# Performance work log

Hardware: AMD Instinct MI355X
Metric: run time of the kernel (lower is better)

Reference implementation:

```python
import jax, jax.numpy as jnp
import numpy as np
from jax import lax

B, T, C = 32, 512, 128
K = 3                      # top_k periods
MIN_P, MAX_P = 8, 64       # period search band
P_MAX = MAX_P              # grid width
CYC_MAX = (T + MIN_P - 1) // MIN_P
KW = 9                     # cyc-axis depthwise kernel
GN_G = 32                  # _best_gn_groups(128)
EPS_GN = 1e-5
EPS_ORTH = 1e-6
EPS_W = 1e-8


def setup_inputs() -> dict:
    key = jax.random.key(0)
    ks = jax.random.split(key, 4)
    return {
        "x": jax.random.normal(ks[0], (B, T, C), jnp.float32),
        "W_dw": jax.random.normal(ks[1], (C, 1, KW), jnp.float32) * 0.1,
        "W_pw": jax.random.normal(ks[2], (C, C), jnp.float32) * (1.0 / np.sqrt(C)),
        "gn_weight": jnp.ones((C,), jnp.float32),
        "gn_bias": jnp.zeros((C,), jnp.float32),
        "W_gate": jax.random.normal(ks[3], (C, C), jnp.float32) * (1.0 / np.sqrt(C)),
        "gamma": jnp.full((C,), 1e-3, jnp.float32),
    }


def _autocorr_topk(x):
    # x: [B,T,C] -> period idx [B,K], softmax weights [B,K]
    Xf = jnp.fft.rfft(x, axis=1)
    Pm = (Xf * jnp.conj(Xf)).real.mean(-1)          # [B, T//2+1]
    r = jnp.fft.irfft(Pm, n=T, axis=1)              # [B, T] autocorrelation
    lag = jnp.arange(T)
    valid = (lag >= MIN_P) & (lag <= MAX_P)
    very_neg = jnp.finfo(x.dtype).min / 8
    rm = jnp.where(valid[None, :], r, very_neg)
    vals, idx = lax.top_k(rm, K)
    w = jax.nn.softmax(vals, axis=1)
    return idx, w


def _fold(s, p):
    # s: [N,T,C], p: [N] int periods -> Z [N,C,CYC_MAX,P_MAX], mask, unfold index maps
    N = s.shape[0]
    p = jnp.maximum(p, 1)
    tpad = ((T + p - 1) // p) * p                   # [N]
    cyc = jnp.arange(CYC_MAX)[None, :, None]
    pos = jnp.arange(P_MAX)[None, None, :]
    time = cyc * p[:, None, None] + pos             # [N,CYC_MAX,P_MAX]
    valid = (pos < p[:, None, None]) & (time < tpad[:, None, None])
    # right-side reflect padding indices
    m = 2 * (T - 1)
    rr = time % m
    src_idx = jnp.where(rr < T, rr, m - rr)
    src = jnp.take_along_axis(s, src_idx.reshape(N, -1)[:, :, None], axis=1)
    src = src.reshape(N, CYC_MAX, P_MAX, C) * valid[..., None].astype(s.dtype)
    Z = jnp.transpose(src, (0, 3, 1, 2))            # [N,C,CYC_MAX,P_MAX]
    mask2d = valid[:, None].astype(s.dtype)         # [N,1,CYC_MAX,P_MAX]
    t = jnp.arange(T)[None, :]
    cyc_T = jnp.clip(t // p[:, None], 0, CYC_MAX - 1)
    pos_T = jnp.clip(t % p[:, None], 0, P_MAX - 1)
    return Z, mask2d, cyc_T, pos_T


def _cyc_conv(Z, mask2d, W_dw, W_pw, gn_w, gn_b, W_gate, gamma):
    # CycAxisConv1d: mean over period axis, depthwise+pointwise conv along cyc,
    # GroupNorm, GELU, SE-gate, LayerScale residual broadcast back to 2D.
    N, _, L, _ = Z.shape
    u = Z.mean(-1)                                  # [N,C,L]
    h = lax.conv_general_dilated(u, W_dw, (1,), [(KW // 2, KW // 2)],
                                 dimension_numbers=('NCH', 'OIH', 'NCH'),
                                 feature_group_count=C)
    h = jnp.einsum('oc,ncl->nol', W_pw, h)
    hg = h.reshape(N, GN_G, C // GN_G, L)
    mean = hg.mean((2, 3), keepdims=True)
    var = hg.var((2, 3), keepdims=True)
    hg = (hg - mean) * lax.rsqrt(var + EPS_GN)
    h = hg.reshape(N, C, L) * gn_w[None, :, None] + gn_b[None, :, None]
    h = jax.nn.gelu(h, approximate=False)
    gate = jax.nn.sigmoid(jnp.einsum('oc,nc->no', W_gate, u.mean(-1)))
    h = h * gate[:, :, None]
    x2d = h[..., None] * gamma[None, :, None, None] * mask2d
    return Z + x2d


def _unfold(Z, cyc_T, pos_T):
    N = Z.shape[0]
    Zf = Z.reshape(N, C, CYC_MAX * P_MAX)
    sp = jnp.clip(cyc_T * P_MAX + pos_T, 0, CYC_MAX * P_MAX - 1)  # [N,T]
    y = jnp.take_along_axis(Zf, sp[:, None, :], axis=2)           # [N,C,T]
    return jnp.transpose(y, (0, 2, 1))                            # [N,T,C]


def reference(x, W_dw, W_pw, gn_weight, gn_bias, W_gate, gamma):
    idx, w = _autocorr_topk(x)                      # [B,K], [B,K]
    p_flat = idx.reshape(-1)                        # [B*K]
    s = jnp.repeat(x, K, axis=0)                    # [B*K,T,C]
    Z, mask2d, cyc_T, pos_T = _fold(s, p_flat)
    Z = _cyc_conv(Z, mask2d, W_dw, W_pw, gn_weight, gn_bias, W_gate, gamma)
    y = _unfold(Z, cyc_T, pos_T).reshape(B, K, T, C)
    periodic = jnp.einsum('bk,bktc->btc', w, y)
    # period confidence Gamma from weight entropy
    H = -(w * jnp.log(w + EPS_W)).sum(1)
    Gamma = jnp.clip(1.0 - H / (jnp.log(float(K) + EPS_W) + EPS_W), 0.0, 1.0)
    # orthogonal residual of local part against periodic part
    local = x - periodic
    num = (local * periodic).sum(1, keepdims=True)
    den = (periodic * periodic).sum(1, keepdims=True) + EPS_ORTH
    local_orth = local - num / den * periodic
    g = Gamma[:, None, None]
    return g * (periodic + local_orth) + (1.0 - g) * x
```

## Files before the change

### kernel.cpp

```cpp
#include <hip/hip_runtime.h>
#include <math.h>

static constexpr int Bn   = 32;
static constexpr int Tn   = 512;
static constexpr int Cn   = 128;
static constexpr int Kk   = 3;
static constexpr int NLAG = 57;
static constexpr int CYC  = 64;
static constexpr int KWn  = 9;

__global__ __launch_bounds__(256) void k_autocorr(const float* __restrict__ x,
    float* __restrict__ r_ws) {
  const int b   = blockIdx.x >> 3;
  const int grp = blockIdx.x & 7;
  const int L0  = 8 + grp * 8;
  const int tid = threadIdx.x;
  const float4* X4 = (const float4*)(x + (size_t)b * Tn * Cn);

  float acc[8];
#pragma unroll
  for (int i = 0; i < 8; ++i) acc[i] = 0.f;

  for (int it = 0; it < 8; ++it) {
    const int id = it * 256 + tid;
    const int c4 = id & 31;
    const int t0 = (id >> 5) * 8;
    float4 A[8];
#pragma unroll
    for (int j = 0; j < 8; ++j) A[j] = X4[(t0 + j) * 32 + c4];
    float4 R[16];
#pragma unroll
    for (int j = 0; j < 16; ++j) R[j] = X4[((t0 + L0 + j) & 511) * 32 + c4];
#pragma unroll
    for (int g = 0; g < 8; ++g) {
#pragma unroll
      for (int j = 0; j < 8; ++j) {
        const float4 a = A[j];
        const float4 r = R[g + j];
        acc[g] += a.x * r.x + a.y * r.y + a.z * r.z + a.w * r.w;
      }
    }
  }

  __shared__ float lds_r[4][8];
  const int lane = tid & 63, wave = tid >> 6;
#pragma unroll
  for (int g = 0; g < 8; ++g) {
    float v = acc[g];
#pragma unroll
    for (int m = 32; m > 0; m >>= 1) v += __shfl_xor(v, m, 64);
    if (lane == 0) lds_r[wave][g] = v;
  }
  __syncthreads();
  if (tid < 8) {
    const int li = grp * 8 + tid;
    if (li < NLAG) {
      r_ws[b * NLAG + li] =
          (lds_r[0][tid] + lds_r[1][tid] + lds_r[2][tid] + lds_r[3][tid]) * (1.0f / Cn);
    }
  }
}

__global__ __launch_bounds__(64) void k_topk(const float* __restrict__ r_ws,
    int* __restrict__ p_idx, float* __restrict__ wv, float* __restrict__ gval) {
  const int b = blockIdx.x;
  const int tid = threadIdx.x;
  __shared__ float rs[NLAG];
  if (tid < NLAG) rs[tid] = r_ws[b * NLAG + tid];
  __syncthreads();
  if (tid == 0) {
    float tmp[NLAG];
    for (int i = 0; i < NLAG; ++i) tmp[i] = rs[i];
    float vals[Kk]; int lags[Kk];
    for (int k = 0; k < Kk; ++k) {
      float best = -INFINITY; int bi = 0;
      for (int i = 0; i < NLAG; ++i)
        if (tmp[i] > best) { best = tmp[i]; bi = i; }
      vals[k] = best; lags[k] = bi + 8; tmp[bi] = -INFINITY;
    }
    const float m  = vals[0];
    const float e0 = expf(vals[0] - m), e1 = expf(vals[1] - m), e2 = expf(vals[2] - m);
    const float s  = e0 + e1 + e2;
    const float w0 = e0 / s, w1 = e1 / s, w2 = e2 / s;
    p_idx[b * 3 + 0] = lags[0]; p_idx[b * 3 + 1] = lags[1]; p_idx[b * 3 + 2] = lags[2];
    wv[b * 3 + 0] = w0; wv[b * 3 + 1] = w1; wv[b * 3 + 2] = w2;
    const float H  = -(w0 * logf(w0 + 1e-8f) + w1 * logf(w1 + 1e-8f) + w2 * logf(w2 + 1e-8f));
    const float lg = logf(3.0f + 1e-8f) + 1e-8f;
    float G = 1.0f - H / lg;
    gval[b] = fminf(fmaxf(G, 0.0f), 1.0f);
  }
}

__global__ __launch_bounds__(128) void k_fold_u(const float* __restrict__ x,
    const int* __restrict__ p_idx, float* __restrict__ u) {
  const int l = blockIdx.x;
  const int n = blockIdx.y;
  const int c = threadIdx.x;
  const int p = p_idx[n];
  const int ncyc = (Tn + p - 1) / p;
  float acc = 0.f;
  if (l < ncyc) {
    const float* xb = x + (size_t)(n / 3) * Tn * Cn;
    const int base = l * p;
    for (int j = 0; j < p; ++j) {
      const int time = base + j;
      const int src = time < Tn ? time : (2 * (Tn - 1) - time);
      acc += xb[src * Cn + c];
    }
  }
  u[((size_t)n * CYC + l) * Cn + c] = acc * (1.0f / 64.0f);
}

__global__ __launch_bounds__(256) void k_cycconv(
    const float* __restrict__ u, const float* __restrict__ Wdw,
    const float* __restrict__ Wpw, const float* __restrict__ gnw,
    const float* __restrict__ gnb, const float* __restrict__ Wgate,
    float* __restrict__ hh) {
  const int n  = blockIdx.x;
  const int og = blockIdx.y;
  const int tid = threadIdx.x;
  const int l  = tid & 63;
  const int wq = __builtin_amdgcn_readfirstlane(tid >> 6);

  __shared__ float smem[8320];
  __shared__ float ubar_s[Cn];
  __shared__ float gates_s[16];

  const float* un = u + (size_t)n * CYC * Cn;

  for (int i = 0; i < 32; ++i) {
    const int idx = i * 256 + tid;
    const int ll = idx >> 7, cc = idx & 127;
    smem[ll * 129 + cc] = un[idx];
  }
  __syncthreads();

  if (tid < Cn) {
    float s = 0.f;
    for (int ll = 0; ll < CYC; ++ll) s += smem[ll * 129 + tid];
    ubar_s[tid] = s * (1.0f / CYC);
  }

  float hreg[32];
  {
    const int c0 = wq * 32;
#pragma unroll
    for (int i = 0; i < 32; ++i) {
      const int c = c0 + i;
      float s = 0.f;
#pragma unroll
      for (int k = 0; k < KWn; ++k) {
        const int ll = l + k - KWn / 2;
        if (ll >= 0 && ll < CYC) s += smem[ll * 129 + c] * Wdw[c * KWn + k];
      }
      hreg[i] = s;
    }
  }
  __syncthreads();

  if (tid < 16) {
    const int o = og * 16 + tid;
    float z = 0.f;
    for (int c = 0; c < Cn; ++c) z += Wgate[o * Cn + c] * ubar_s[c];
    gates_s[tid] = 1.0f / (1.0f + expf(-z));
  }

  {
    const int c0 = wq * 32;
#pragma unroll
    for (int i = 0; i < 32; ++i) smem[(c0 + i) * 65 + l] = hreg[i];
  }
  __syncthreads();

  const int o4 = og * 16 + wq * 4;
  float acc[4];
#pragma unroll
  for (int i = 0; i < 4; ++i) acc[i] = 0.f;
  const float* wb = Wpw + (size_t)o4 * Cn;
  for (int c = 0; c < Cn; ++c) {
    const float hv = smem[c * 65 + l];
#pragma unroll
    for (int i = 0; i < 4; ++i) acc[i] = fmaf(wb[i * Cn + c], hv, acc[i]);
  }

  float s1 = acc[0] + acc[1] + acc[2] + acc[3];
  float s2 = acc[0]*acc[0] + acc[1]*acc[1] + acc[2]*acc[2] + acc[3]*acc[3];
#pragma unroll
  for (int m = 32; m > 0; m >>= 1) {
    s1 += __shfl_xor(s1, m, 64);
    s2 += __shfl_xor(s2, m, 64);
  }
  const float mean = s1 * (1.0f / 256.0f);
  const float var  = s2 * (1.0f / 256.0f) - mean * mean;
  const float rstd = rsqrtf(var + 1e-5f);

  float4 res;
  float* rp = (float*)&res;
#pragma unroll
  for (int i = 0; i < 4; ++i) {
    const int o = o4 + i;
    float h = (acc[i] - mean) * rstd;
    h = h * gnw[o] + gnb[o];
    h = 0.5f * h * (1.0f + erff(h * 0.70710678118654752440f));
    rp[i] = h * gates_s[o - og * 16];
  }
  *(float4*)(hh + (size_t)n * CYC * Cn + l * Cn + o4) = res;
}

__global__ __launch_bounds__(128) void k_dot(const float* __restrict__ x,
    const float* __restrict__ hh, const int* __restrict__ p_idx,
    const float* __restrict__ wv, const float* __restrict__ gamma,
    float* __restrict__ pna, float* __restrict__ pda) {
  const int q = blockIdx.x, b = blockIdx.y;
  const int tid = threadIdx.x;
  const int t0 = q * 64;
  __shared__ unsigned short cycs[64][4];

  const int p0 = p_idx[b * 3 + 0], p1 = p_idx[b * 3 + 1], p2 = p_idx[b * 3 + 2];
  const float w0 = wv[b * 3 + 0], w1 = wv[b * 3 + 1], w2 = wv[b * 3 + 2];
  const float sw = w0 + w1 + w2;
  if (tid < 64) {
    const int t = t0 + tid;
    cycs[tid][0] = (unsigned short)(t / p0);
    cycs[tid][1] = (unsigned short)(t / p1);
    cycs[tid][2] = (unsigned short)(t / p2);
  }
  __syncthreads();

  const int c = tid;
  const float gam = gamma[c];
  const float* hh0 = hh + ((size_t)(b * 3 + 0) * CYC) * Cn + c;
  const float* hh1 = hh + ((size_t)(b * 3 + 1) * CYC) * Cn + c;
  const float* hh2 = hh + ((size_t)(b * 3 + 2) * CYC) * Cn + c;
  const float* xb = x + (size_t)b * Tn * Cn;

  float na = 0.f, da = 0.f;
  for (int tt = 0; tt < 64; ++tt) {
    const int t = t0 + tt;
    const float xv = xb[t * Cn + c];
    const float dv = gam * (w0 * hh0[cycs[tt][0] * Cn] +
                            w1 * hh1[cycs[tt][1] * Cn] +
                            w2 * hh2[cycs[tt][2] * Cn]);
    const float P = sw * xv + dv;
    na += (xv - P) * P;
    da += P * P;
  }
  pna[((size_t)b * 8 + q) * Cn + c] = na;
  pda[((size_t)b * 8 + q) * Cn + c] = da;
}

__global__ __launch_bounds__(128) void k_out(const float* __restrict__ x,
    const float* __restrict__ hh, const int* __restrict__ p_idx,
    const float* __restrict__ wv, const float* __restrict__ gval,
    const float* __restrict__ gamma, const float* __restrict__ pna,
    const float* __restrict__ pda, float* __restrict__ out) {
  const int q = blockIdx.x, b = blockIdx.y;
  const int tid = threadIdx.x;
  const int t0 = q * 64;
  __shared__ unsigned short cycs[64][4];

  const int p0 = p_idx[b * 3 + 0], p1 = p_idx[b * 3 + 1], p2 = p_idx[b * 3 + 2];
  const float w0 = wv[b * 3 + 0], w1 = wv[b * 3 + 1], w2 = wv[b * 3 + 2];
  const float sw = w0 + w1 + w2;
  const float g = gval[b];
  if (tid < 64) {
    const int t = t0 + tid;
    cycs[tid][0] = (unsigned short)(t / p0);
    cycs[tid][1] = (unsigned short)(t / p1);
    cycs[tid][2] = (unsigned short)(t / p2);
  }
  __syncthreads();

  const int c = tid;
  float num = 0.f, den = 1e-6f;
#pragma unroll
  for (int qq = 0; qq < 8; ++qq) {
    num += pna[((size_t)b * 8 + qq) * Cn + c];
    den += pda[((size_t)b * 8 + qq) * Cn + c];
  }
  const float sc = g * (num / den);

  const float gam = gamma[c];
  const float* hh0 = hh + ((size_t)(b * 3 + 0) * CYC) * Cn + c;
  const float* hh1 = hh + ((size_t)(b * 3 + 1) * CYC) * Cn + c;
  const float* hh2 = hh + ((size_t)(b * 3 + 2) * CYC) * Cn + c;
  const float* xb = x + (size_t)b * Tn * Cn;
  float* ob = out + (size_t)b * Tn * Cn;

  for (int tt = 0; tt < 64; ++tt) {
    const int t = t0 + tt;
    const float xv = xb[t * Cn + c];
    const float dv = gam * (w0 * hh0[cycs[tt][0] * Cn] +
                            w1 * hh1[cycs[tt][1] * Cn] +
                            w2 * hh2[cycs[tt][2] * Cn]);
    const float P = sw * xv + dv;
    ob[t * Cn + c] = xv - sc * P;
  }
}

extern "C" void kernel_launch(void* const* d_in, const int* in_sizes, int n_in,
                              void* d_out, int out_size, void* d_ws, size_t ws_size,
                              hipStream_t stream) {
  const float* x     = (const float*)d_in[0];
  const float* Wdw   = (const float*)d_in[1];
  const float* Wpw   = (const float*)d_in[2];
  const float* gnw   = (const float*)d_in[3];
  const float* gnb   = (const float*)d_in[4];
  const float* Wgate = (const float*)d_in[5];
  const float* gamma = (const float*)d_in[6];
  float* out = (float*)d_out;

  char* ws = (char*)d_ws;
  int*   p_idx = (int*)ws;
  float* wvp   = (float*)(ws + 512);
  float* gvalp = (float*)(ws + 1024);
  float* r_ws  = (float*)(ws + 2048);
  float* pna   = (float*)(ws + 10240);
  float* pda   = (float*)(ws + 10240 + 131072);
  float* u     = (float*)(ws + 10240 + 262144);
  float* hh    = (float*)(ws + 10240 + 262144 + 3145728);

  k_autocorr<<<Bn * 8, 256, 0, stream>>>(x, r_ws);
  k_topk<<<Bn, 64, 0, stream>>>(r_ws, p_idx, wvp, gvalp);
  k_fold_u<<<dim3(CYC, Bn * Kk), 128, 0, stream>>>(x, p_idx, u);
  k_cycconv<<<dim3(Bn * Kk, 8), 256, 0, stream>>>(u, Wdw, Wpw, gnw, gnb, Wgate, hh);
  k_dot<<<dim3(8, Bn), 128, 0, stream>>>(x, hh, p_idx, wvp, gamma, pna, pda);
  k_out<<<dim3(8, Bn), 128, 0, stream>>>(x, hh, p_idx, wvp, gvalp, gamma, pna, pda, out);
}
```

Before: 165.0 us.

## Fuse topk and fold into consumers, split autocorr over time for more blocks

```diff
diff --git a/kernel.cpp b/kernel.cpp
--- a/kernel.cpp
+++ b/kernel.cpp
@@ -9,10 +9,35 @@
 static constexpr int CYC  = 64;
 static constexpr int KWn  = 9;
 
-__global__ __launch_bounds__(256) void k_autocorr(const float* __restrict__ x,
+__device__ __forceinline__ void topk_scan(const float* __restrict__ r_ws, int b,
+    int& p0, int& p1, int& p2, float& w0, float& w1, float& w2, float& Gv) {
+  const float* r0 = r_ws + (size_t)(b * 4 + 0) * NLAG;
+  const float* r1 = r_ws + (size_t)(b * 4 + 1) * NLAG;
+  const float* r2 = r_ws + (size_t)(b * 4 + 2) * NLAG;
+  const float* r3 = r_ws + (size_t)(b * 4 + 3) * NLAG;
+  float v0 = -INFINITY, v1 = -INFINITY, v2 = -INFINITY;
+  int i0 = 0, i1 = 0, i2 = 0;
+  for (int i = 0; i < NLAG; ++i) {
+    const float v = r0[i] + r1[i] + r2[i] + r3[i];
+    if (v > v0)      { v2 = v1; i2 = i1; v1 = v0; i1 = i0; v0 = v; i0 = i; }
+    else if (v > v1) { v2 = v1; i2 = i1; v1 = v; i1 = i; }
+    else if (v > v2) { v2 = v; i2 = i; }
+  }
+  p0 = i0 + 8; p1 = i1 + 8; p2 = i2 + 8;
+  const float e1 = expf(v1 - v0), e2 = expf(v2 - v0);
+  const float s = 1.0f + e1 + e2;
+  w0 = 1.0f / s; w1 = e1 / s; w2 = e2 / s;
+  const float H  = -(w0 * logf(w0 + 1e-8f) + w1 * logf(w1 + 1e-8f) + w2 * logf(w2 + 1e-8f));
+  const float lg = logf(3.0f + 1e-8f) + 1e-8f;
+  Gv = fminf(fmaxf(1.0f - H / lg, 0.0f), 1.0f);
+}
+
+__global__ __launch_bounds__(256, 3) void k_autocorr(const float* __restrict__ x,
     float* __restrict__ r_ws) {
-  const int b   = blockIdx.x >> 3;
-  const int grp = blockIdx.x & 7;
+  const int bk  = blockIdx.x;
+  const int b   = bk >> 5;
+  const int grp = (bk >> 2) & 7;
+  const int th  = bk & 3;
   const int L0  = 8 + grp * 8;
   const int tid = threadIdx.x;
   const float4* X4 = (const float4*)(x + (size_t)b * Tn * Cn);
@@ -21,8 +46,9 @@
 #pragma unroll
   for (int i = 0; i < 8; ++i) acc[i] = 0.f;
 
-  for (int it = 0; it < 8; ++it) {
-    const int id = it * 256 + tid;
+#pragma unroll
+  for (int s = 0; s < 2; ++s) {
+    const int id = (th * 2 + s) * 256 + tid;
     const int c4 = id & 31;
     const int t0 = (id >> 5) * 8;
     float4 A[8];
@@ -55,83 +81,53 @@
   if (tid < 8) {
     const int li = grp * 8 + tid;
     if (li < NLAG) {
-      r_ws[b * NLAG + li] =
+      r_ws[(size_t)(b * 4 + th) * NLAG + li] =
           (lds_r[0][tid] + lds_r[1][tid] + lds_r[2][tid] + lds_r[3][tid]) * (1.0f / Cn);
     }
   }
 }
 
-__global__ __launch_bounds__(64) void k_topk(const float* __restrict__ r_ws,
-    int* __restrict__ p_idx, float* __restrict__ wv, float* __restrict__ gval) {
-  const int b = blockIdx.x;
-  const int tid = threadIdx.x;
-  __shared__ float rs[NLAG];
-  if (tid < NLAG) rs[tid] = r_ws[b * NLAG + tid];
-  __syncthreads();
-  if (tid == 0) {
-    float tmp[NLAG];
-    for (int i = 0; i < NLAG; ++i) tmp[i] = rs[i];
-    float vals[Kk]; int lags[Kk];
-    for (int k = 0; k < Kk; ++k) {
-      float best = -INFINITY; int bi = 0;
-      for (int i = 0; i < NLAG; ++i)
-        if (tmp[i] > best) { best = tmp[i]; bi = i; }
-      vals[k] = best; lags[k] = bi + 8; tmp[bi] = -INFINITY;
-    }
-    const float m  = vals[0];
-    const float e0 = expf(vals[0] - m), e1 = expf(vals[1] - m), e2 = expf(vals[2] - m);
-    const float s  = e0 + e1 + e2;
-    const float w0 = e0 / s, w1 = e1 / s, w2 = e2 / s;
-    p_idx[b * 3 + 0] = lags[0]; p_idx[b * 3 + 1] = lags[1]; p_idx[b * 3 + 2] = lags[2];
-    wv[b * 3 + 0] = w0; wv[b * 3 + 1] = w1; wv[b * 3 + 2] = w2;
-    const float H  = -(w0 * logf(w0 + 1e-8f) + w1 * logf(w1 + 1e-8f) + w2 * logf(w2 + 1e-8f));
-    const float lg = logf(3.0f + 1e-8f) + 1e-8f;
-    float G = 1.0f - H / lg;
-    gval[b] = fminf(fmaxf(G, 0.0f), 1.0f);
-  }
-}
-
-__global__ __launch_bounds__(128) void k_fold_u(const float* __restrict__ x,
-    const int* __restrict__ p_idx, float* __restrict__ u) {
-  const int l = blockIdx.x;
-  const int n = blockIdx.y;
-  const int c = threadIdx.x;
-  const int p = p_idx[n];
-  const int ncyc = (Tn + p - 1) / p;
-  float acc = 0.f;
-  if (l < ncyc) {
-    const float* xb = x + (size_t)(n / 3) * Tn * Cn;
-    const int base = l * p;
-    for (int j = 0; j < p; ++j) {
-      const int time = base + j;
-      const int src = time < Tn ? time : (2 * (Tn - 1) - time);
-      acc += xb[src * Cn + c];
-    }
-  }
-  u[((size_t)n * CYC + l) * Cn + c] = acc * (1.0f / 64.0f);
-}
-
-__global__ __launch_bounds__(256) void k_cycconv(
-    const float* __restrict__ u, const float* __restrict__ Wdw,
+__global__ __launch_bounds__(256) void k_foldconv(const float* __restrict__ x,
+    const float* __restrict__ r_ws, const float* __restrict__ Wdw,
     const float* __restrict__ Wpw, const float* __restrict__ gnw,
     const float* __restrict__ gnb, const float* __restrict__ Wgate,
     float* __restrict__ hh) {
   const int n  = blockIdx.x;
   const int og = blockIdx.y;
+  const int b  = n / 3;
+  const int kk = n - b * 3;
   const int tid = threadIdx.x;
   const int l  = tid & 63;
-  const int wq = __builtin_amdgcn_readfirstlane(tid >> 6);
+
+  int p0, p1, p2; float w0, w1, w2, Gv;
+  topk_scan(r_ws, b, p0, p1, p2, w0, w1, w2, Gv);
+  const int p = (kk == 0) ? p0 : ((kk == 1) ? p1 : p2);
+  const int ncyc = (Tn + p - 1) / p;
 
   __shared__ float smem[8320];
   __shared__ float ubar_s[Cn];
   __shared__ float gates_s[16];
 
-  const float* un = u + (size_t)n * CYC * Cn;
-
-  for (int i = 0; i < 32; ++i) {
-    const int idx = i * 256 + tid;
-    const int ll = idx >> 7, cc = idx & 127;
-    smem[ll * 129 + cc] = un[idx];
+  const float4* X4 = (const float4*)(x + (size_t)b * Tn * Cn);
+  for (int it = 0; it < 8; ++it) {
+    const int id = it * 256 + tid;
+    const int c4 = id & 31;
+    const int ll = id >> 5;
+    float sx = 0.f, sy = 0.f, sz = 0.f, sw2 = 0.f;
+    if (ll < ncyc) {
+      const int base = ll * p;
+      for (int j = 0; j < p; ++j) {
+        const int time = base + j;
+        const int src = time < Tn ? time : (2 * (Tn - 1) - time);
+        const float4 a = X4[src * 32 + c4];
+        sx += a.x; sy += a.y; sz += a.z; sw2 += a.w;
+      }
+    }
+    const int adr = ll * 129 + c4 * 4;
+    smem[adr + 0] = sx * (1.0f / 64.0f);
+    smem[adr + 1] = sy * (1.0f / 64.0f);
+    smem[adr + 2] = sz * (1.0f / 64.0f);
+    smem[adr + 3] = sw2 * (1.0f / 64.0f);
   }
   __syncthreads();
 
@@ -142,40 +138,32 @@
   }
 
   float hreg[32];
-  {
-    const int c0 = wq * 32;
-#pragma unroll
-    for (int i = 0; i < 32; ++i) {
-      const int c = c0 + i;
-      float s = 0.f;
-#pragma unroll
-      for (int k = 0; k < KWn; ++k) {
-        const int ll = l + k - KWn / 2;
-        if (ll >= 0 && ll < CYC) s += smem[ll * 129 + c] * Wdw[c * KWn + k];
-      }
-      hreg[i] = s;
+  const int c0 = (tid >> 6) * 32;
+#pragma unroll
+  for (int i = 0; i < 32; ++i) {
+    const int c = c0 + i;
+    float s = 0.f;
+#pragma unroll
+    for (int k2 = 0; k2 < KWn; ++k2) {
+      const int ll = l + k2 - KWn / 2;
+      if (ll >= 0 && ll < CYC) s += smem[ll * 129 + c] * Wdw[c * KWn + k2];
     }
-  }
-  __syncthreads();
-
+    hreg[i] = s;
+  }
+  __syncthreads();
+
+#pragma unroll
+  for (int i = 0; i < 32; ++i) smem[(c0 + i) * 65 + l] = hreg[i];
   if (tid < 16) {
     const int o = og * 16 + tid;
     float z = 0.f;
     for (int c = 0; c < Cn; ++c) z += Wgate[o * Cn + c] * ubar_s[c];
     gates_s[tid] = 1.0f / (1.0f + expf(-z));
   }
-
-  {
-    const int c0 = wq * 32;
-#pragma unroll
-    for (int i = 0; i < 32; ++i) smem[(c0 + i) * 65 + l] = hreg[i];
-  }
-  __syncthreads();
-
-  const int o4 = og * 16 + wq * 4;
-  float acc[4];
-#pragma unroll
-  for (int i = 0; i < 4; ++i) acc[i] = 0.f;
+  __syncthreads();
+
+  const int o4 = og * 16 + (tid >> 6) * 4;
+  float acc[4] = {0.f, 0.f, 0.f, 0.f};
   const float* wb = Wpw + (size_t)o4 * Cn;
   for (int c = 0; c < Cn; ++c) {
     const float hv = smem[c * 65 + l];
@@ -204,20 +192,20 @@
     h = 0.5f * h * (1.0f + erff(h * 0.70710678118654752440f));
     rp[i] = h * gates_s[o - og * 16];
   }
-  *(float4*)(hh + (size_t)n * CYC * Cn + l * Cn + o4) = res;
+  *(float4*)(hh + ((size_t)n * CYC + l) * Cn + o4) = res;
 }
 
 __global__ __launch_bounds__(128) void k_dot(const float* __restrict__ x,
-    const float* __restrict__ hh, const int* __restrict__ p_idx,
-    const float* __restrict__ wv, const float* __restrict__ gamma,
-    float* __restrict__ pna, float* __restrict__ pda) {
+    const float* __restrict__ hh, const float* __restrict__ r_ws,
+    const float* __restrict__ gamma, float* __restrict__ pna,
+    float* __restrict__ pda) {
   const int q = blockIdx.x, b = blockIdx.y;
   const int tid = threadIdx.x;
   const int t0 = q * 64;
   __shared__ unsigned short cycs[64][4];
 
-  const int p0 = p_idx[b * 3 + 0], p1 = p_idx[b * 3 + 1], p2 = p_idx[b * 3 + 2];
-  const float w0 = wv[b * 3 + 0], w1 = wv[b * 3 + 1], w2 = wv[b * 3 + 2];
+  int p0, p1, p2; float w0, w1, w2, Gv;
+  topk_scan(r_ws, b, p0, p1, p2, w0, w1, w2, Gv);
   const float sw = w0 + w1 + w2;
   if (tid < 64) {
     const int t = t0 + tid;
@@ -250,8 +238,7 @@
 }
 
 __global__ __launch_bounds__(128) void k_out(const float* __restrict__ x,
-    const float* __restrict__ hh, const int* __restrict__ p_idx,
-    const float* __restrict__ wv, const float* __restrict__ gval,
+    const float* __restrict__ hh, const float* __restrict__ r_ws,
     const float* __restrict__ gamma, const float* __restrict__ pna,
     const float* __restrict__ pda, float* __restrict__ out) {
   const int q = blockIdx.x, b = blockIdx.y;
@@ -259,10 +246,9 @@
   const int t0 = q * 64;
   __shared__ unsigned short cycs[64][4];
 
-  const int p0 = p_idx[b * 3 + 0], p1 = p_idx[b * 3 + 1], p2 = p_idx[b * 3 + 2];
-  const float w0 = wv[b * 3 + 0], w1 = wv[b * 3 + 1], w2 = wv[b * 3 + 2];
+  int p0, p1, p2; float w0, w1, w2, Gv;
+  topk_scan(r_ws, b, p0, p1, p2, w0, w1, w2, Gv);
   const float sw = w0 + w1 + w2;
-  const float g = gval[b];
   if (tid < 64) {
     const int t = t0 + tid;
     cycs[tid][0] = (unsigned short)(t / p0);
@@ -278,7 +264,7 @@
     num += pna[((size_t)b * 8 + qq) * Cn + c];
     den += pda[((size_t)b * 8 + qq) * Cn + c];
   }
-  const float sc = g * (num / den);
+  const float sc = Gv * (num / den);
 
   const float gam = gamma[c];
   const float* hh0 = hh + ((size_t)(b * 3 + 0) * CYC) * Cn + c;
@@ -311,19 +297,13 @@
   float* out = (float*)d_out;
 
   char* ws = (char*)d_ws;
-  int*   p_idx = (int*)ws;
-  float* wvp   = (float*)(ws + 512);
-  float* gvalp = (float*)(ws + 1024);
-  float* r_ws  = (float*)(ws + 2048);
-  float* pna   = (float*)(ws + 10240);
-  float* pda   = (float*)(ws + 10240 + 131072);
-  float* u     = (float*)(ws + 10240 + 262144);
-  float* hh    = (float*)(ws + 10240 + 262144 + 3145728);
-
-  k_autocorr<<<Bn * 8, 256, 0, stream>>>(x, r_ws);
-  k_topk<<<Bn, 64, 0, stream>>>(r_ws, p_idx, wvp, gvalp);
-  k_fold_u<<<dim3(CYC, Bn * Kk), 128, 0, stream>>>(x, p_idx, u);
-  k_cycconv<<<dim3(Bn * Kk, 8), 256, 0, stream>>>(u, Wdw, Wpw, gnw, gnb, Wgate, hh);
-  k_dot<<<dim3(8, Bn), 128, 0, stream>>>(x, hh, p_idx, wvp, gamma, pna, pda);
-  k_out<<<dim3(8, Bn), 128, 0, stream>>>(x, hh, p_idx, wvp, gvalp, gamma, pna, pda, out);
-}
+  float* r_ws = (float*)ws;
+  float* pna  = (float*)(ws + 65536);
+  float* pda  = (float*)(ws + 65536 + 131072);
+  float* hh   = (float*)(ws + 1048576);
+
+  k_autocorr<<<Bn * 32, 256, 0, stream>>>(x, r_ws);
+  k_foldconv<<<dim3(Bn * Kk, 8), 256, 0, stream>>>(x, r_ws, Wdw, Wpw, gnw, gnb, Wgate, hh);
+  k_dot<<<dim3(8, Bn), 128, 0, stream>>>(x, hh, r_ws, gamma, pna, pda);
+  k_out<<<dim3(8, Bn), 128, 0, stream>>>(x, hh, r_ws, gamma, pna, pda, out);
+}
```

Result: slower. 199.7 us (+21.0%).
